# Performance work log

Hardware: AMD Instinct MI355X
Metric: run time of the kernel (lower is better)

## Reference

```python
import jax, jax.numpy as jnp
import numpy as np

B, S, D, H = 2, 2048, 1024, 16
DH = D // H


def _rel_shift(pos_score):
    # pos_score: [B,H,S,S] -> Transformer-XL relative shift via pad/reshape/slice
    b, h, s1, s2 = pos_score.shape
    zeros = jnp.zeros((b, h, s1, 1), dtype=pos_score.dtype)
    padded = jnp.concatenate([zeros, pos_score], axis=-1)          # [B,H,S1,S2+1]
    padded = padded.reshape(b, h, s2 + 1, s1)                       # [B,H,S2+1,S1]
    return padded[:, :, 1:].reshape(b, h, s1, s2)


def setup_inputs() -> dict:
    key = jax.random.key(0)
    ks = jax.random.split(key, 16)
    sc = 0.02
    return {
        "q": jax.random.normal(ks[0], (B, S, D), jnp.float32),
        "k": jax.random.normal(ks[1], (B, S, D), jnp.float32),
        "v": jax.random.normal(ks[2], (B, S, D), jnp.float32),
        "pos_embedding": jax.random.normal(ks[3], (B, S, D), jnp.float32),
        "Wq": jax.random.normal(ks[4], (D, D), jnp.float32) * sc,
        "bq": jnp.zeros((D,), jnp.float32),
        "Wk": jax.random.normal(ks[5], (D, D), jnp.float32) * sc,
        "bk": jnp.zeros((D,), jnp.float32),
        "Wv": jax.random.normal(ks[6], (D, D), jnp.float32) * sc,
        "bv": jnp.zeros((D,), jnp.float32),
        "Wp": jax.random.normal(ks[7], (D, D), jnp.float32) * sc,
        "u_bias": jax.random.normal(ks[8], (H, DH), jnp.float32) * sc,
        "v_bias": jax.random.normal(ks[9], (H, DH), jnp.float32) * sc,
        "Wo": jax.random.normal(ks[10], (D, D), jnp.float32) * sc,
        "bo": jnp.zeros((D,), jnp.float32),
    }


def reference(q, k, v, pos_embedding, Wq, bq, Wk, bk, Wv, bv, Wp, u_bias, v_bias, Wo, bo):
    b = q.shape[0]
    qh = (q @ Wq.T + bq).reshape(b, -1, H, DH)          # [B,S,H,dh]
    kh = (k @ Wk.T + bk).reshape(b, -1, H, DH)
    vh = (v @ Wv.T + bv).reshape(b, -1, H, DH)
    ph = (pos_embedding @ Wp.T).reshape(b, -1, H, DH)    # pos Linear has no bias
    content = jnp.einsum('bqhd,bkhd->bhqk', qh + u_bias, kh)
    pos = jnp.einsum('bqhd,bkhd->bhqk', qh + v_bias, ph)
    pos = _rel_shift(pos)
    score = (content + pos) / jnp.sqrt(jnp.float32(D))   # scaled by sqrt(d_model), as in source
    attn = jax.nn.softmax(score, axis=-1)                # dropout p=0 -> identity
    out = jnp.einsum('bhqk,bkhd->bqhd', attn, vh).reshape(b, -1, D)
    return out @ Wo.T + bo
```

## Files before the change

kernel.cpp:

```cpp
#include <hip/hip_runtime.h>

#define B_ 2
#define S_ 2048
#define D_ 1024
#define H_ 16
#define DH_ 64

typedef unsigned short u16;
typedef short v8s __attribute__((ext_vector_type(8)));
typedef float v4f __attribute__((ext_vector_type(4)));

__device__ __forceinline__ u16 f2bf(float x) {
    unsigned int u = __float_as_uint(x);
    u += 0x7fffu + ((u >> 16) & 1u);
    return (u16)(u >> 16);
}
__device__ __forceinline__ float bf2f(u16 u) {
    return __uint_as_float(((unsigned int)u) << 16);
}

typedef __attribute__((address_space(1))) void gvoid;
typedef __attribute__((address_space(3))) void lvoid;
#define CP16(g, l) __builtin_amdgcn_global_load_lds((gvoid*)(g), (lvoid*)(l), 16, 0, 0)

__global__ __launch_bounds__(256) void cvt9(
    const float* __restrict__ s0, const float* __restrict__ s1,
    const float* __restrict__ s2, const float* __restrict__ s3,
    const float* __restrict__ s4, const float* __restrict__ s5,
    const float* __restrict__ s6, const float* __restrict__ s7,
    const float* __restrict__ s8,
    u16* __restrict__ d0, u16* __restrict__ d1, u16* __restrict__ d2,
    u16* __restrict__ d3, u16* __restrict__ d4, u16* __restrict__ d5,
    u16* __restrict__ d6, u16* __restrict__ d7, u16* __restrict__ d8,
    int nbig, int nsmall)
{
    int y = blockIdx.y;
    const float* s = y==0?s0:y==1?s1:y==2?s2:y==3?s3:y==4?s4:y==5?s5:y==6?s6:y==7?s7:s8;
    u16* d = y==0?d0:y==1?d1:y==2?d2:y==3?d3:y==4?d4:y==5?d5:y==6?d6:y==7?d7:d8;
    int n4 = (y < 4) ? nbig : nsmall;
    int i = blockIdx.x * 256 + threadIdx.x;
    if (i < n4) {
        float4 v = ((const float4*)s)[i];
        ushort4 o;
        o.x = f2bf(v.x); o.y = f2bf(v.y); o.z = f2bf(v.z); o.w = f2bf(v.w);
        ((ushort4*)d)[i] = o;
    }
}

__global__ __launch_bounds__(256, 3) void gemm_proj(
    const u16* __restrict__ A0, const u16* __restrict__ A1,
    const u16* __restrict__ A2, const u16* __restrict__ A3,
    const u16* __restrict__ W0, const u16* __restrict__ W1,
    const u16* __restrict__ W2, const u16* __restrict__ W3,
    const float* __restrict__ b0, const float* __restrict__ b1,
    const float* __restrict__ b2,
    u16* __restrict__ C0, u16* __restrict__ C1,
    u16* __restrict__ VT, u16* __restrict__ C3)
{
    const int K = D_, N = D_;
    const int proj = blockIdx.z;
    const u16* A = proj==0?A0:proj==1?A1:proj==2?A2:A3;
    const u16* W = proj==0?W0:proj==1?W1:proj==2?W2:W3;
    const float* bias = proj==0?b0:proj==1?b1:proj==2?b2:nullptr;

    __shared__ u16 As[128 * 64];
    __shared__ u16 Ws[128 * 64];
    const int tid  = threadIdx.x;
    const int wave = tid >> 6, lane = tid & 63;
    const int quad = lane >> 4, l15 = lane & 15;
    const int m0 = blockIdx.y * 128, n0 = blockIdx.x * 128;
    const int wr = wave >> 1, wc = wave & 1;

    const int lr8 = lane >> 3;
    const int lc8 = ((lane & 7) ^ lr8) * 8;
    const int ksw = (l15 & 7) * 8;

    v4f acc[4][4];
    #pragma unroll
    for (int i = 0; i < 4; ++i)
        #pragma unroll
        for (int j = 0; j < 4; ++j) acc[i][j] = (v4f){0.f, 0.f, 0.f, 0.f};

    for (int kb = 0; kb < K; kb += 64) {
        __syncthreads();
        #pragma unroll
        for (int c = 0; c < 4; ++c) {
            int seg = wave * 4 + c;
            CP16(A + (size_t)(m0 + seg * 8 + lr8) * K + kb + lc8, &As[seg * 512]);
            CP16(W + (size_t)(n0 + seg * 8 + lr8) * K + kb + lc8, &Ws[seg * 512]);
        }
        __syncthreads();
        #pragma unroll
        for (int kk = 0; kk < 2; ++kk) {
            v8s af[4], bf[4];
            #pragma unroll
            for (int i = 0; i < 4; ++i)
                af[i] = *(const v8s*)&As[(wr * 64 + i * 16 + l15) * 64 + ((kk * 32 + quad * 8) ^ ksw)];
            #pragma unroll
            for (int j = 0; j < 4; ++j)
                bf[j] = *(const v8s*)&Ws[(wc * 64 + j * 16 + l15) * 64 + ((kk * 32 + quad * 8) ^ ksw)];
            #pragma unroll
            for (int i = 0; i < 4; ++i)
                #pragma unroll
                for (int j = 0; j < 4; ++j)
                    acc[i][j] = __builtin_amdgcn_mfma_f32_16x16x32_bf16(af[i], bf[j], acc[i][j], 0, 0, 0);
        }
    }

    float bb[4];
    #pragma unroll
    for (int j = 0; j < 4; ++j)
        bb[j] = bias ? bias[n0 + wc * 64 + j * 16 + l15] : 0.f;

    if (proj == 2) {
        #pragma unroll
        for (int i = 0; i < 4; ++i)
            #pragma unroll
            for (int j = 0; j < 4; ++j) {
                int r0 = m0 + wr * 64 + i * 16 + quad * 4;
                int c  = n0 + wc * 64 + j * 16 + l15;
                ushort4 pw;
                pw.x = f2bf(acc[i][j][0] + bb[j]);
                pw.y = f2bf(acc[i][j][1] + bb[j]);
                pw.z = f2bf(acc[i][j][2] + bb[j]);
                pw.w = f2bf(acc[i][j][3] + bb[j]);
                size_t row_vt = (size_t)((r0 >> 11) * 16 + (c >> 6)) * 64 + (c & 63);
                *(ushort4*)&VT[row_vt * S_ + (r0 & 2047)] = pw;
            }
    } else {
        u16* C = proj == 0 ? C0 : proj == 1 ? C1 : C3;
        #pragma unroll
        for (int i = 0; i < 4; ++i)
            #pragma unroll
            for (int j = 0; j < 4; ++j)
                #pragma unroll
                for (int reg = 0; reg < 4; ++reg) {
                    int r = m0 + wr * 64 + i * 16 + quad * 4 + reg;
                    int c = n0 + wc * 64 + j * 16 + l15;
                    C[(size_t)r * N + c] = f2bf(acc[i][j][reg] + bb[j]);
                }
    }
}

__global__ __launch_bounds__(256, 3) void gemm_out(
    const u16* __restrict__ A, const u16* __restrict__ W,
    const float* __restrict__ bias, float* __restrict__ C)
{
    const int K = D_, N = D_;
    __shared__ u16 As[64 * 32];
    __shared__ u16 Ws[128 * 32];
    const int tid  = threadIdx.x;
    const int wave = tid >> 6, lane = tid & 63;
    const int quad = lane >> 4, l15 = lane & 15;
    const int m0 = blockIdx.y * 64, n0 = blockIdx.x * 128;
    const int srow = lane >> 2, scol = (lane & 3) * 8;
    const int wr = wave >> 1, wc = wave & 1;

    v4f acc[2][4];
    #pragma unroll
    for (int i = 0; i < 2; ++i)
        #pragma unroll
        for (int j = 0; j < 4; ++j) acc[i][j] = (v4f){0.f, 0.f, 0.f, 0.f};

    for (int kb = 0; kb < K; kb += 32) {
        __syncthreads();
        CP16(A + (size_t)(m0 + wave * 16 + srow) * K + kb + scol, &As[wave * 512]);
        CP16(W + (size_t)(n0 + wave * 16 + srow) * K + kb + scol, &Ws[wave * 512]);
        CP16(W + (size_t)(n0 + (wave + 4) * 16 + srow) * K + kb + scol, &Ws[(wave + 4) * 512]);
        __syncthreads();
        v8s af[2], bf[4];
        #pragma unroll
        for (int i = 0; i < 2; ++i)
            af[i] = *(const v8s*)&As[(wr * 32 + i * 16 + l15) * 32 + quad * 8];
        #pragma unroll
        for (int j = 0; j < 4; ++j)
            bf[j] = *(const v8s*)&Ws[(wc * 64 + j * 16 + l15) * 32 + quad * 8];
        #pragma unroll
        for (int i = 0; i < 2; ++i)
            #pragma unroll
            for (int j = 0; j < 4; ++j)
                acc[i][j] = __builtin_amdgcn_mfma_f32_16x16x32_bf16(af[i], bf[j], acc[i][j], 0, 0, 0);
    }

    #pragma unroll
    for (int i = 0; i < 2; ++i)
        #pragma unroll
        for (int j = 0; j < 4; ++j)
            #pragma unroll
            for (int reg = 0; reg < 4; ++reg) {
                int r = m0 + wr * 32 + i * 16 + quad * 4 + reg;
                int c = n0 + wc * 64 + j * 16 + l15;
                C[(size_t)r * N + c] = acc[i][j][reg] + bias[c];
            }
}

__global__ __launch_bounds__(256)
__attribute__((amdgpu_waves_per_eu(4, 4)))
void rel_attn13(
    const u16* __restrict__ QH, const u16* __restrict__ KH,
    const u16* __restrict__ VT, const u16* __restrict__ PH,
    const float* __restrict__ ub, const float* __restrict__ vb,
    u16* __restrict__ AO)
{
    __shared__ u16 Ks[64 * 64];
    __shared__ u16 VTs[64 * 64];
    __shared__ u16 PmT[4][80][16];
    __shared__ u16 ps[4][16][40];

    const int tid  = threadIdx.x;
    const int wave = tid >> 6, lane = tid & 63;
    const int quad = lane >> 4, l15 = lane & 15;

    const int wg  = blockIdx.x + 32 * blockIdx.y;
    const int xcd = wg & 7;
    const int i2  = wg >> 3;
    const int bh  = xcd + 8 * (i2 & 3);
    const int xt  = i2 >> 2;

    const int q0 = (xt * 4 + wave) * 16;
    const int bb = bh >> 4, h = bh & 15;
    const size_t base = (size_t)bb * S_ * D_ + (size_t)h * DH_;
    const size_t vtb  = (size_t)bh * DH_ * S_;

    const int lr8 = lane >> 3;
    const int lc8 = ((lane & 7) ^ lr8) * 8;
    const int ksw = (l15 & 7) * 8;

    v8s quf[2], qvf0[2], qvf1[2];
    #pragma unroll
    for (int kc = 0; kc < 2; ++kc) {
        int r0 = q0 + l15;
        int r1 = min(r0 + 1, S_ - 1);
        v8s raw0 = *(const v8s*)&QH[base + (size_t)r0 * D_ + kc * 32 + quad * 8];
        v8s raw1 = *(const v8s*)&QH[base + (size_t)r1 * D_ + kc * 32 + quad * 8];
        #pragma unroll
        for (int j = 0; j < 8; ++j) {
            float ubj = ub[h * DH_ + kc * 32 + quad * 8 + j];
            float vbj = vb[h * DH_ + kc * 32 + quad * 8 + j];
            float f0 = bf2f((u16)raw0[j]);
            quf[kc][j]  = (short)f2bf(f0 + ubj);
            qvf0[kc][j] = (short)f2bf(f0 + vbj);
            qvf1[kc][j] = (short)f2bf(bf2f((u16)raw1[j]) + vbj);
        }
    }

    v4f o[4];
    float l_r[4];
    #pragma unroll
    for (int i = 0; i < 4; ++i) { o[i] = (v4f){0.f, 0.f, 0.f, 0.f}; l_r[i] = 0.f; }

    const int wb = l15 - quad * 4 + 15;

    auto body = [&](int k0, const int phase) {
        __syncthreads();

        #pragma unroll
        for (int c = 0; c < 2; ++c) {
            int seg = wave * 2 + c;
            CP16(KH + base + (size_t)(k0 + seg * 8 + lr8) * D_ + lc8, &Ks[seg * 512]);
            CP16(VT + vtb + (size_t)(seg * 8 + lr8) * S_ + k0 + lc8, &VTs[seg * 512]);
        }

        const int tmin = k0 - q0 - 15;
        const int jbase = (phase == 0) ? (S_ - 1 + tmin) : (tmin - 2);

        auto phaddr = [&](int wcl) -> const u16* {
            int rw = wcl * 16 + l15;
            int j;
            if (phase == 1) {
                int t = tmin + rw;
                j = (t <= 0) ? (S_ - 1 + t) : max(t - 2, 0);
            } else {
                j = jbase + rw;
            }
            return &PH[base + (size_t)j * D_ + quad * 8];
        };

        {
            const u16* ph0 = phaddr(0);
            v8s p0 = *(const v8s*)ph0;
            v8s p1 = *(const v8s*)(ph0 + 32);
            const bool doA = (tmin <= 0);
            #pragma unroll
            for (int wcl = 0; wcl < 5; ++wcl) {
                v8s n0, n1;
                if (wcl < 4) {
                    const u16* phn = phaddr(wcl + 1);
                    n0 = *(const v8s*)phn;
                    n1 = *(const v8s*)(phn + 32);
                }
                int rw = wcl * 16 + l15;
                v4f sel;
                if (phase == 1) {
                    int t = tmin + rw;
                    v4f a1 = (v4f){0.f, 0.f, 0.f, 0.f};
                    a1 = __builtin_amdgcn_mfma_f32_16x16x32_bf16(qvf1[0], p0, a1, 0, 0, 0);
                    a1 = __builtin_amdgcn_mfma_f32_16x16x32_bf16(qvf1[1], p1, a1, 0, 0, 0);
                    sel = a1;
                    if (doA) {
                        v4f a0 = (v4f){0.f, 0.f, 0.f, 0.f};
                        a0 = __builtin_amdgcn_mfma_f32_16x16x32_bf16(qvf0[0], p0, a0, 0, 0, 0);
                        a0 = __builtin_amdgcn_mfma_f32_16x16x32_bf16(qvf0[1], p1, a0, 0, 0, 0);
                        sel = (t >= 2) ? a1 : a0;
                    }
                } else {
                    const v8s a0s = (phase == 0) ? qvf0[0] : qvf1[0];
                    const v8s a1s = (phase == 0) ? qvf0[1] : qvf1[1];
                    v4f a = (v4f){0.f, 0.f, 0.f, 0.f};
                    a = __builtin_amdgcn_mfma_f32_16x16x32_bf16(a0s, p0, a, 0, 0, 0);
                    a = __builtin_amdgcn_mfma_f32_16x16x32_bf16(a1s, p1, a, 0, 0, 0);
                    sel = a;
                }
                ushort4 pw;
                pw.x = f2bf(sel[0]); pw.y = f2bf(sel[1]); pw.z = f2bf(sel[2]); pw.w = f2bf(sel[3]);
                *(ushort4*)&PmT[wave][rw][quad * 4] = pw;
                p0 = n0; p1 = n1;
            }
        }

        __syncthreads();

        #pragma unroll
        for (int hf = 0; hf < 2; ++hf) {
            #pragma unroll
            for (int c2 = 0; c2 < 2; ++c2) {
                int ct = hf * 2 + c2;
                int kr = (ct * 16 + l15) * 64;
                v8s kbf0 = *(const v8s*)&Ks[kr + ((quad * 8) ^ ksw)];
                v8s kbf1 = *(const v8s*)&Ks[kr + ((32 + quad * 8) ^ ksw)];
                v4f cs = (v4f){0.f, 0.f, 0.f, 0.f};
                cs = __builtin_amdgcn_mfma_f32_16x16x32_bf16(quf[0], kbf0, cs, 0, 0, 0);
                cs = __builtin_amdgcn_mfma_f32_16x16x32_bf16(quf[1], kbf1, cs, 0, 0, 0);
                #pragma unroll
                for (int reg = 0; reg < 4; ++reg) {
                    int qrow = quad * 4 + reg;
                    int wcol = ct * 16 + wb - reg;
                    float pos = bf2f(PmT[wave][wcol][qrow]);
                    if (phase == 1) {
                        int t = tmin + wcol;
                        if (t == 1) pos = 0.f;
                    }
                    float e = __expf((cs[reg] + pos) * 0.03125f);
                    ps[wave][qrow][c2 * 16 + l15] = f2bf(e);
                    l_r[reg] += e;
                }
            }
            v8s af = *(const v8s*)&ps[wave][l15][quad * 8];
            #pragma unroll
            for (int dt = 0; dt < 4; ++dt) {
                int vr = (dt * 16 + l15) * 64;
                v8s vbf = *(const v8s*)&VTs[vr + ((hf * 32 + quad * 8) ^ ksw)];
                o[dt] = __builtin_amdgcn_mfma_f32_16x16x32_bf16(af, vbf, o[dt], 0, 0, 0);
            }
        }
    };

    const int k1end   = (q0 >= 63) ? ((((q0 - 63) >> 6) + 1) << 6) : 0;
    const int k2start = min((((q0 + 80) >> 6) << 6), S_);

    int k0 = 0;
    for (; k0 < k1end; k0 += 64)   body(k0, 0);
    for (; k0 < k2start; k0 += 64) body(k0, 1);
    for (; k0 < S_; k0 += 64)      body(k0, 2);

    #pragma unroll
    for (int reg = 0; reg < 4; ++reg) {
        float s = l_r[reg];
        #pragma unroll
        for (int off = 1; off < 16; off <<= 1)
            s += __shfl_xor(s, off, 16);
        l_r[reg] = 1.f / s;
    }
    #pragma unroll
    for (int dt = 0; dt < 4; ++dt)
        #pragma unroll
        for (int reg = 0; reg < 4; ++reg)
            AO[base + (size_t)(q0 + quad * 4 + reg) * D_ + dt * 16 + l15] =
                f2bf(o[dt][reg] * l_r[reg]);
}

extern "C" void kernel_launch(void* const* d_in, const int* in_sizes, int n_in,
                              void* d_out, int out_size, void* d_ws, size_t ws_size,
                              hipStream_t stream)
{
    (void)in_sizes; (void)n_in; (void)out_size; (void)ws_size;
    const float* q   = (const float*)d_in[0];
    const float* k   = (const float*)d_in[1];
    const float* v   = (const float*)d_in[2];
    const float* pe  = (const float*)d_in[3];
    const float* Wq  = (const float*)d_in[4];
    const float* bq  = (const float*)d_in[5];
    const float* Wk  = (const float*)d_in[6];
    const float* bk  = (const float*)d_in[7];
    const float* Wv  = (const float*)d_in[8];
    const float* bv  = (const float*)d_in[9];
    const float* Wp  = (const float*)d_in[10];
    const float* ub  = (const float*)d_in[11];
    const float* vbs = (const float*)d_in[12];
    const float* Wo  = (const float*)d_in[13];
    const float* bo  = (const float*)d_in[14];
    float* out = (float*)d_out;

    const size_t NSD = (size_t)B_ * S_ * D_;
    const size_t DD  = (size_t)D_ * D_;
    u16* ws = (u16*)d_ws;
    u16* qB  = ws;
    u16* kB  = qB + NSD;
    u16* vB  = kB + NSD;
    u16* pB  = vB + NSD;
    u16* WqB = pB + NSD;
    u16* WkB = WqB + DD;
    u16* WvB = WkB + DD;
    u16* WpB = WvB + DD;
    u16* WoB = WpB + DD;
    u16* QH  = WoB + DD;
    u16* KH  = QH + NSD;
    u16* VT  = KH + NSD;
    u16* PHb = VT + NSD;
    u16* AO  = qB;

    const int M = B_ * S_;

    cvt9<<<dim3((int)(NSD / 4 / 256), 9), 256, 0, stream>>>(
        q, k, v, pe, Wq, Wk, Wv, Wp, Wo,
        qB, kB, vB, pB, WqB, WkB, WvB, WpB, WoB,
        (int)(NSD / 4), (int)(DD / 4));

    gemm_proj<<<dim3(D_ / 128, M / 128, 4), 256, 0, stream>>>(
        qB, kB, vB, pB, WqB, WkB, WvB, WpB, bq, bk, bv, QH, KH, VT, PHb);

    rel_attn13<<<dim3(S_ / 64, B_ * H_), 256, 0, stream>>>(QH, KH, VT, PHb, ub, vbs, AO);

    gemm_out<<<dim3(D_ / 128, M / 64), 256, 0, stream>>>(AO, WoB, bo, out);
}
```

Before: 396.6 us.

## Deepen out-projection K tile with swizzled LDS and restructure attention P·V staging

The output GEMM now stages 64-wide K slices instead of 32-wide, with an XOR-swizzled LDS layout. This halves the number of barrier pairs per K loop and aims to avoid bank conflicts. The attention kernel computes all four score tiles into a wider per-wave probability buffer before running P·V once per 64-key block, not once per half. It also pads PmT and ps to change the LDS bank mapping. The cost is more LDS per block, which may reduce occupancy, and somewhat more live registers in the attention inner loop.

```diff
diff --git a/kernel.cpp b/kernel.cpp
--- a/kernel.cpp
+++ b/kernel.cpp
@@ -147,39 +147,52 @@
     const float* __restrict__ bias, float* __restrict__ C)
 {
     const int K = D_, N = D_;
-    __shared__ u16 As[64 * 32];
-    __shared__ u16 Ws[128 * 32];
+    __shared__ u16 As[64 * 64];
+    __shared__ u16 Ws[128 * 64];
     const int tid  = threadIdx.x;
     const int wave = tid >> 6, lane = tid & 63;
     const int quad = lane >> 4, l15 = lane & 15;
     const int m0 = blockIdx.y * 64, n0 = blockIdx.x * 128;
-    const int srow = lane >> 2, scol = (lane & 3) * 8;
     const int wr = wave >> 1, wc = wave & 1;
 
+    const int lr8 = lane >> 3;
+    const int lc8 = ((lane & 7) ^ lr8) * 8;
+    const int ksw = (l15 & 7) * 8;
+
     v4f acc[2][4];
     #pragma unroll
     for (int i = 0; i < 2; ++i)
         #pragma unroll
         for (int j = 0; j < 4; ++j) acc[i][j] = (v4f){0.f, 0.f, 0.f, 0.f};
 
-    for (int kb = 0; kb < K; kb += 32) {
-        __syncthreads();
-        CP16(A + (size_t)(m0 + wave * 16 + srow) * K + kb + scol, &As[wave * 512]);
-        CP16(W + (size_t)(n0 + wave * 16 + srow) * K + kb + scol, &Ws[wave * 512]);
-        CP16(W + (size_t)(n0 + (wave + 4) * 16 + srow) * K + kb + scol, &Ws[(wave + 4) * 512]);
-        __syncthreads();
-        v8s af[2], bf[4];
-        #pragma unroll
-        for (int i = 0; i < 2; ++i)
-            af[i] = *(const v8s*)&As[(wr * 32 + i * 16 + l15) * 32 + quad * 8];
-        #pragma unroll
-        for (int j = 0; j < 4; ++j)
-            bf[j] = *(const v8s*)&Ws[(wc * 64 + j * 16 + l15) * 32 + quad * 8];
-        #pragma unroll
-        for (int i = 0; i < 2; ++i)
+    for (int kb = 0; kb < K; kb += 64) {
+        __syncthreads();
+        #pragma unroll
+        for (int c = 0; c < 2; ++c) {
+            int seg = wave * 2 + c;
+            CP16(A + (size_t)(m0 + seg * 8 + lr8) * K + kb + lc8, &As[seg * 512]);
+        }
+        #pragma unroll
+        for (int c = 0; c < 4; ++c) {
+            int seg = wave * 4 + c;
+            CP16(W + (size_t)(n0 + seg * 8 + lr8) * K + kb + lc8, &Ws[seg * 512]);
+        }
+        __syncthreads();
+        #pragma unroll
+        for (int kk = 0; kk < 2; ++kk) {
+            v8s af[2], bf[4];
+            #pragma unroll
+            for (int i = 0; i < 2; ++i)
+                af[i] = *(const v8s*)&As[(wr * 32 + i * 16 + l15) * 64 + ((kk * 32 + quad * 8) ^ ksw)];
             #pragma unroll
             for (int j = 0; j < 4; ++j)
-                acc[i][j] = __builtin_amdgcn_mfma_f32_16x16x32_bf16(af[i], bf[j], acc[i][j], 0, 0, 0);
+                bf[j] = *(const v8s*)&Ws[(wc * 64 + j * 16 + l15) * 64 + ((kk * 32 + quad * 8) ^ ksw)];
+            #pragma unroll
+            for (int i = 0; i < 2; ++i)
+                #pragma unroll
+                for (int j = 0; j < 4; ++j)
+                    acc[i][j] = __builtin_amdgcn_mfma_f32_16x16x32_bf16(af[i], bf[j], acc[i][j], 0, 0, 0);
+        }
     }
 
     #pragma unroll
@@ -196,7 +209,7 @@
 
 __global__ __launch_bounds__(256)
 __attribute__((amdgpu_waves_per_eu(4, 4)))
-void rel_attn13(
+void rel_attn15(
     const u16* __restrict__ QH, const u16* __restrict__ KH,
     const u16* __restrict__ VT, const u16* __restrict__ PH,
     const float* __restrict__ ub, const float* __restrict__ vb,
@@ -204,8 +217,8 @@
 {
     __shared__ u16 Ks[64 * 64];
     __shared__ u16 VTs[64 * 64];
-    __shared__ u16 PmT[4][80][16];
-    __shared__ u16 ps[4][16][40];
+    __shared__ u16 PmT[4][80][20];
+    __shared__ u16 ps[4][16][72];
 
     const int tid  = threadIdx.x;
     const int wave = tid >> 6, lane = tid & 63;
@@ -321,37 +334,37 @@
         __syncthreads();
 
         #pragma unroll
-        for (int hf = 0; hf < 2; ++hf) {
-            #pragma unroll
-            for (int c2 = 0; c2 < 2; ++c2) {
-                int ct = hf * 2 + c2;
-                int kr = (ct * 16 + l15) * 64;
-                v8s kbf0 = *(const v8s*)&Ks[kr + ((quad * 8) ^ ksw)];
-                v8s kbf1 = *(const v8s*)&Ks[kr + ((32 + quad * 8) ^ ksw)];
-                v4f cs = (v4f){0.f, 0.f, 0.f, 0.f};
-                cs = __builtin_amdgcn_mfma_f32_16x16x32_bf16(quf[0], kbf0, cs, 0, 0, 0);
-                cs = __builtin_amdgcn_mfma_f32_16x16x32_bf16(quf[1], kbf1, cs, 0, 0, 0);
-                #pragma unroll
-                for (int reg = 0; reg < 4; ++reg) {
-                    int qrow = quad * 4 + reg;
-                    int wcol = ct * 16 + wb - reg;
-                    float pos = bf2f(PmT[wave][wcol][qrow]);
-                    if (phase == 1) {
-                        int t = tmin + wcol;
-                        if (t == 1) pos = 0.f;
-                    }
-                    float e = __expf((cs[reg] + pos) * 0.03125f);
-                    ps[wave][qrow][c2 * 16 + l15] = f2bf(e);
-                    l_r[reg] += e;
+        for (int ct = 0; ct < 4; ++ct) {
+            int kr = (ct * 16 + l15) * 64;
+            v8s kbf0 = *(const v8s*)&Ks[kr + ((quad * 8) ^ ksw)];
+            v8s kbf1 = *(const v8s*)&Ks[kr + ((32 + quad * 8) ^ ksw)];
+            v4f cs = (v4f){0.f, 0.f, 0.f, 0.f};
+            cs = __builtin_amdgcn_mfma_f32_16x16x32_bf16(quf[0], kbf0, cs, 0, 0, 0);
+            cs = __builtin_amdgcn_mfma_f32_16x16x32_bf16(quf[1], kbf1, cs, 0, 0, 0);
+            #pragma unroll
+            for (int reg = 0; reg < 4; ++reg) {
+                int qrow = quad * 4 + reg;
+                int wcol = ct * 16 + wb - reg;
+                float pos = bf2f(PmT[wave][wcol][qrow]);
+                if (phase == 1) {
+                    int t = tmin + wcol;
+                    if (t == 1) pos = 0.f;
                 }
+                float e = __expf((cs[reg] + pos) * 0.03125f);
+                ps[wave][qrow][ct * 16 + l15] = f2bf(e);
+                l_r[reg] += e;
             }
-            v8s af = *(const v8s*)&ps[wave][l15][quad * 8];
-            #pragma unroll
-            for (int dt = 0; dt < 4; ++dt) {
-                int vr = (dt * 16 + l15) * 64;
-                v8s vbf = *(const v8s*)&VTs[vr + ((hf * 32 + quad * 8) ^ ksw)];
-                o[dt] = __builtin_amdgcn_mfma_f32_16x16x32_bf16(af, vbf, o[dt], 0, 0, 0);
-            }
+        }
+
+        v8s af0 = *(const v8s*)&ps[wave][l15][quad * 8];
+        v8s af1 = *(const v8s*)&ps[wave][l15][32 + quad * 8];
+        #pragma unroll
+        for (int dt = 0; dt < 4; ++dt) {
+            int vr = (dt * 16 + l15) * 64;
+            v8s vbf0 = *(const v8s*)&VTs[vr + ((quad * 8) ^ ksw)];
+            v8s vbf1 = *(const v8s*)&VTs[vr + ((32 + quad * 8) ^ ksw)];
+            o[dt] = __builtin_amdgcn_mfma_f32_16x16x32_bf16(af0, vbf0, o[dt], 0, 0, 0);
+            o[dt] = __builtin_amdgcn_mfma_f32_16x16x32_bf16(af1, vbf1, o[dt], 0, 0, 0);
         }
     };
 
@@ -429,7 +442,7 @@
     gemm_proj<<<dim3(D_ / 128, M / 128, 4), 256, 0, stream>>>(
         qB, kB, vB, pB, WqB, WkB, WvB, WpB, bq, bk, bv, QH, KH, VT, PHb);
 
-    rel_attn13<<<dim3(S_ / 64, B_ * H_), 256, 0, stream>>>(QH, KH, VT, PHb, ub, vbs, AO);
+    rel_attn15<<<dim3(S_ / 64, B_ * H_), 256, 0, stream>>>(QH, KH, VT, PHb, ub, vbs, AO);
 
     gemm_out<<<dim3(D_ / 128, M / 64), 256, 0, stream>>>(AO, WoB, bo, out);
 }
```

New measurement: 385.9 us. -2.7%, faster.
